# Kernel optimization log

Hardware: AMD Instinct MI355X
Metric: run time of the kernel (lower is better)

The kernel has to match this reference:

```python
import jax, jax.numpy as jnp
import numpy as np
import math

N, E, G = 20000, 160000, 256
H, L, R, LAT, TD = 128, 4, 64, 128, 64
CUT = 6.0
NTYPES = 101  # max_atomic_num=100 -> 101 rows, row 0 is padding


def _lin(key, fan_in, fan_out):
    kw, _ = jax.random.split(key)
    w = jax.random.normal(kw, (fan_in, fan_out), jnp.float32) / np.sqrt(fan_in).astype(np.float32)
    b = jnp.zeros((fan_out,), jnp.float32)
    return w, b


def _stack_lin(key, fan_in, fan_out):
    keys = jax.random.split(key, L)
    ws, bs = zip(*[_lin(k, fan_in, fan_out) for k in keys])
    return jnp.stack(ws), jnp.stack(bs)


def setup_inputs() -> dict:
    key = jax.random.key(0)
    ks = list(jax.random.split(key, 24))
    noisy_coords = jax.random.uniform(ks[0], (N, 3), jnp.float32)
    noisy_types = jax.random.randint(ks[1], (N,), 0, NTYPES)
    z = jax.random.normal(ks[2], (G, LAT), jnp.float32)
    t = jax.random.uniform(ks[3], (G,), jnp.float32) * 1000.0
    edge_index = jax.random.randint(ks[4], (2, E), 0, N)
    batch = jnp.sort(jax.random.randint(ks[5], (N,), 0, G))
    lattice = jnp.eye(3, dtype=jnp.float32)[None] * 5.0 + 0.1 * jax.random.normal(ks[6], (G, 3, 3), jnp.float32)
    offsets = jax.random.randint(ks[7], (E, 3), -1, 2).astype(jnp.float32)
    atom_embed = jax.random.normal(ks[8], (NTYPES, H), jnp.float32) * 0.02
    atom_embed = atom_embed.at[0].set(0.0)  # padding_idx=0
    z_w, z_b = _lin(ks[9], LAT, H)
    t_w, t_b = _lin(ks[10], TD, H)
    msg_w1, msg_b1 = _stack_lin(ks[11], H, H)
    msg_w2, msg_b2 = _stack_lin(ks[12], H, 3 * H)
    rbf_w, rbf_b = _stack_lin(ks[13], R, 3 * H)
    U = jax.random.normal(ks[14], (L, H, H), jnp.float32) / np.sqrt(H).astype(np.float32)
    V = jax.random.normal(ks[15], (L, H, H), jnp.float32) / np.sqrt(H).astype(np.float32)
    upd_w1, upd_b1 = _stack_lin(ks[16], 2 * H, H)
    upd_w2, upd_b2 = _stack_lin(ks[17], H, 3 * H)
    hc_w1, hc_b1 = _lin(ks[18], H, H)
    hc_w2, hc_b2 = _lin(ks[19], H, 3)
    ht_w1, ht_b1 = _lin(ks[20], H, H)
    ht_w2, ht_b2 = _lin(ks[21], H, NTYPES)
    return dict(noisy_coords=noisy_coords, noisy_types=noisy_types, z=z, t=t,
                edge_index=edge_index, batch=batch, lattice=lattice, offsets=offsets,
                atom_embed=atom_embed, z_w=z_w, z_b=z_b, t_w=t_w, t_b=t_b,
                msg_w1=msg_w1, msg_b1=msg_b1, msg_w2=msg_w2, msg_b2=msg_b2,
                rbf_w=rbf_w, rbf_b=rbf_b, U=U, V=V,
                upd_w1=upd_w1, upd_b1=upd_b1, upd_w2=upd_w2, upd_b2=upd_b2,
                hc_w1=hc_w1, hc_b1=hc_b1, hc_w2=hc_w2, hc_b2=hc_b2,
                ht_w1=ht_w1, ht_b1=ht_b1, ht_w2=ht_w2, ht_b2=ht_b2)


def reference(noisy_coords, noisy_types, z, t, edge_index, batch, lattice, offsets,
              atom_embed, z_w, z_b, t_w, t_b,
              msg_w1, msg_b1, msg_w2, msg_b2, rbf_w, rbf_b, U, V,
              upd_w1, upd_b1, upd_w2, upd_b2,
              hc_w1, hc_b1, hc_w2, hc_b2, ht_w1, ht_b1, ht_w2, ht_b2):
    n = noisy_coords.shape[0]
    src, dst = edge_index[0], edge_index[1]

    # node embeddings + conditioning
    s = atom_embed[noisy_types]                       # [N, H]
    v = jnp.zeros((n, 3, H), s.dtype)                 # [N, 3, H]
    half = TD // 2
    freqs = jnp.exp(-math.log(10000.0) * jnp.arange(half, dtype=jnp.float32) / (half - 1))
    emb = t[:, None] * freqs[None, :]                 # [G, TD/2]
    t_emb = jnp.concatenate([jnp.sin(emb), jnp.cos(emb)], axis=-1)  # [G, TD]
    cond = (z @ z_w + z_b)[batch] + (t_emb @ t_w + t_b)[batch]      # [N, H]

    # edge geometry: gather -> diff -> 3x3 matmul -> norm -> RBF -> normalize
    frac_diff = noisy_coords[dst] - noisy_coords[src] + offsets     # [E, 3]
    cart = jnp.einsum('ei,eij->ej', frac_diff, lattice[batch[src]]) # [E, 3]
    dist = jnp.maximum(jnp.sqrt(jnp.sum(cart * cart, -1)), 1e-8)    # clamp(min=1e-8)
    centers = jnp.linspace(0.0, CUT, R)
    gamma = jnp.float32(R / CUT)
    rbf = jnp.exp(-gamma * (dist[:, None] - centers[None, :]) ** 2) # [E, R]
    unit = cart / jnp.maximum(jnp.sqrt(jnp.sum(cart * cart, -1, keepdims=True)), 1e-12)

    # PaiNN layers (canonical message + update blocks)
    for l in range(L):
        s = s + cond
        # message block
        phi = jax.nn.silu(s @ msg_w1[l] + msg_b1[l]) @ msg_w2[l] + msg_b2[l]  # [N, 3H]
        filt = rbf @ rbf_w[l] + rbf_b[l]                                      # [E, 3H]
        x = phi[src] * filt
        ds, dv1, dv2 = jnp.split(x, 3, axis=-1)
        s = s + jax.ops.segment_sum(ds, dst, num_segments=n)
        vmsg = dv1[:, None, :] * v[src] + dv2[:, None, :] * unit[:, :, None]  # [E, 3, H]
        v = v + jax.ops.segment_sum(vmsg, dst, num_segments=n)
        # update block
        Uv = jnp.einsum('nch,hk->nck', v, U[l])
        Vv = jnp.einsum('nch,hk->nck', v, V[l])
        Vn = jnp.sqrt(jnp.sum(Vv * Vv, axis=1) + 1e-8)                        # [N, H]
        a = jax.nn.silu(jnp.concatenate([s, Vn], -1) @ upd_w1[l] + upd_b1[l]) @ upd_w2[l] + upd_b2[l]
        avv, asv, ass = jnp.split(a, 3, axis=-1)
        v = v + avv[:, None, :] * Uv
        s = s + asv * jnp.sum(Uv * Vv, axis=1) + ass

    coords_out = jax.nn.silu(s @ hc_w1 + hc_b1) @ hc_w2 + hc_b2   # [N, 3]
    type_out = jax.nn.silu(s @ ht_w1 + ht_b1) @ ht_w2 + ht_b2     # [N, 101]
    return coords_out, type_out
```

## Files before the change

### kernel.cpp

```cpp
#include <hip/hip_runtime.h>
#include <hip/hip_bf16.h>

#define HD 128
#define RD 64
#define H3 384

typedef float f32x4 __attribute__((ext_vector_type(4)));
typedef unsigned short us8 __attribute__((ext_vector_type(8)));
typedef __bf16 bf16x8 __attribute__((ext_vector_type(8)));

__device__ __forceinline__ float silu_f(float x) {
    return x / (1.0f + __expf(-x));
}
__device__ __forceinline__ unsigned short f2bf(float x) {
    __hip_bfloat16 h = __float2bfloat16(x);
    return *reinterpret_cast<unsigned short*>(&h);
}
__device__ __forceinline__ float bf2f(unsigned short u) {
    return __uint_as_float(((unsigned)u) << 16);
}
__device__ __forceinline__ f32x4 mfma3(us8 ah, us8 al, us8 bh, us8 bl, f32x4 c) {
    bf16x8 AH = __builtin_bit_cast(bf16x8, ah);
    bf16x8 AL = __builtin_bit_cast(bf16x8, al);
    bf16x8 BH = __builtin_bit_cast(bf16x8, bh);
    bf16x8 BL = __builtin_bit_cast(bf16x8, bl);
    c = __builtin_amdgcn_mfma_f32_16x16x32_bf16(AH, BH, c, 0, 0, 0);
    c = __builtin_amdgcn_mfma_f32_16x16x32_bf16(AH, BL, c, 0, 0, 0);
    c = __builtin_amdgcn_mfma_f32_16x16x32_bf16(AL, BH, c, 0, 0, 0);
    return c;
}

__global__ void wprep_kernel(const float* __restrict__ src,
                             unsigned short* __restrict__ dhi, unsigned short* __restrict__ dlo,
                             int K, int OUT, int sStride, int dStride, int nlay) {
    int total = K * OUT;
    for (int idx = blockIdx.x * blockDim.x + threadIdx.x; idx < total * nlay;
         idx += gridDim.x * blockDim.x) {
        int lyr = idx / total, r = idx % total;
        int o = r / K, k = r % K;
        float x = src[(size_t)lyr * sStride + (size_t)k * OUT + o];
        unsigned short hi = f2bf(x);
        unsigned short lo = f2bf(x - bf2f(hi));
        dhi[(size_t)lyr * dStride + (size_t)o * K + k] = hi;
        dlo[(size_t)lyr * dStride + (size_t)o * K + k] = lo;
    }
}

__global__ __launch_bounds__(128) void cond_kernel(const float* __restrict__ z, const float* __restrict__ t,
                            const float* __restrict__ z_w, const float* __restrict__ z_b,
                            const float* __restrict__ t_w, const float* __restrict__ t_b,
                            float* __restrict__ condG) {
    int g = blockIdx.x;
    int k = threadIdx.x;
    __shared__ float zr[128];
    __shared__ float te[64];
    zr[k] = z[g * 128 + k];
    if (k < 32) {
        float f = __expf(-9.2103403719761836f * (float)k / 31.0f);
        float e = t[g] * f;
        te[k] = sinf(e);
        te[32 + k] = cosf(e);
    }
    __syncthreads();
    float acc = z_b[k] + t_b[k];
    #pragma unroll 8
    for (int i = 0; i < 128; ++i) acc += zr[i] * z_w[i * 128 + k];
    #pragma unroll 8
    for (int i = 0; i < 64; ++i) acc += te[i] * t_w[i * 128 + k];
    condG[g * 128 + k] = acc;
}

__global__ void init_kernel(const int* __restrict__ types, const float* __restrict__ emb,
                            const float* __restrict__ condG, const int* __restrict__ batch,
                            float* __restrict__ s, int N_) {
    int i = blockIdx.x * blockDim.x + threadIdx.x;
    if (i < N_ * HD) {
        int n = i >> 7;
        int k = i & 127;
        s[i] = emb[types[n] * HD + k] + condG[batch[n] * 128 + k];
    }
}

__global__ void geom_kernel(const float* __restrict__ coords, const int* __restrict__ srcI,
                            const int* __restrict__ dstI, const int* __restrict__ batch,
                            const float* __restrict__ lattice, const float* __restrict__ offs,
                            float* __restrict__ dist, float* __restrict__ unit, int E_) {
    int e = blockIdx.x * blockDim.x + threadIdx.x;
    if (e >= E_) return;
    int sn = srcI[e], dn = dstI[e];
    float f0 = coords[dn * 3 + 0] - coords[sn * 3 + 0] + offs[e * 3 + 0];
    float f1 = coords[dn * 3 + 1] - coords[sn * 3 + 1] + offs[e * 3 + 1];
    float f2 = coords[dn * 3 + 2] - coords[sn * 3 + 2] + offs[e * 3 + 2];
    const float* Lg = lattice + batch[sn] * 9;
    float c0 = f0 * Lg[0] + f1 * Lg[3] + f2 * Lg[6];
    float c1 = f0 * Lg[1] + f1 * Lg[4] + f2 * Lg[7];
    float c2 = f0 * Lg[2] + f1 * Lg[5] + f2 * Lg[8];
    float nrm = sqrtf(c0 * c0 + c1 * c1 + c2 * c2);
    dist[e] = fmaxf(nrm, 1e-8f);
    float inv = 1.0f / fmaxf(nrm, 1e-12f);
    unit[e * 3 + 0] = c0 * inv;
    unit[e * 3 + 1] = c1 * inv;
    unit[e * 3 + 2] = c2 * inv;
}

__global__ void hist_kernel(const int* __restrict__ dstI, int* __restrict__ cnt, int E_) {
    int e = blockIdx.x * blockDim.x + threadIdx.x;
    if (e < E_) atomicAdd(&cnt[dstI[e]], 1);
}

__global__ __launch_bounds__(1024) void scan_kernel(const int* __restrict__ cnt, int* __restrict__ cur, int n) {
    __shared__ int tmp[1024];
    __shared__ int carry_s;
    if (threadIdx.x == 0) carry_s = 0;
    __syncthreads();
    for (int base = 0; base < n; base += 1024) {
        int i = base + threadIdx.x;
        int x = (i < n) ? cnt[i] : 0;
        tmp[threadIdx.x] = x;
        __syncthreads();
        for (int off = 1; off < 1024; off <<= 1) {
            int y = (threadIdx.x >= off) ? tmp[threadIdx.x - off] : 0;
            __syncthreads();
            tmp[threadIdx.x] += y;
            __syncthreads();
        }
        if (i < n) cur[i] = carry_s + tmp[threadIdx.x] - x;
        __syncthreads();
        if (threadIdx.x == 0) carry_s += tmp[1023];
        __syncthreads();
    }
}

__global__ void scatter_kernel(const int* __restrict__ srcI, const int* __restrict__ dstI,
                               const float* __restrict__ dist, const float* __restrict__ unit,
                               int* __restrict__ cur,
                               float* __restrict__ dist_s, float* __restrict__ unit_s,
                               int* __restrict__ src_s, int* __restrict__ dst_s, int E_) {
    int e = blockIdx.x * blockDim.x + threadIdx.x;
    if (e >= E_) return;
    int d = dstI[e];
    int p = atomicAdd(&cur[d], 1);
    dist_s[p] = dist[e];
    unit_s[p * 3 + 0] = unit[e * 3 + 0];
    unit_s[p * 3 + 1] = unit[e * 3 + 1];
    unit_s[p * 3 + 2] = unit[e * 3 + 2];
    src_s[p] = srcI[e];
    dst_s[p] = d;
}

#define PSA 136
__global__ __launch_bounds__(256, 2) void phi_mfma(
    const float* __restrict__ s,
    const unsigned short* __restrict__ w1h, const unsigned short* __restrict__ w1l,
    const float* __restrict__ b1,
    const unsigned short* __restrict__ w2h, const unsigned short* __restrict__ w2l,
    const float* __restrict__ b2,
    float* __restrict__ phi, int N_) {
    __shared__ unsigned short Ah[32 * PSA], Al[32 * PSA], Hh[32 * PSA], Hl[32 * PSA];
    const int tid = threadIdx.x;
    const int n0 = blockIdx.x * 32;
    for (int idx = tid; idx < 32 * 128; idx += 256) {
        int j = idx >> 7, k = idx & 127;
        int n = n0 + j; if (n >= N_) n = N_ - 1;
        float x = s[(size_t)n * 128 + k];
        unsigned short h = f2bf(x);
        Ah[j * PSA + k] = h;
        Al[j * PSA + k] = f2bf(x - bf2f(h));
    }
    __syncthreads();
    const int w = tid >> 6, l = tid & 63;
    const int lr = l & 15, lk = (l >> 4) << 3, rg0 = (l >> 4) << 2;
    const f32x4 zero4 = {0.0f, 0.0f, 0.0f, 0.0f};
    f32x4 acc1[2][2];
    #pragma unroll
    for (int rt = 0; rt < 2; ++rt)
        #pragma unroll
        for (int ci = 0; ci < 2; ++ci) acc1[rt][ci] = zero4;
    #pragma unroll
    for (int kt = 0; kt < 4; ++kt) {
        int kk = kt * 32 + lk;
        us8 bh[2], bl[2], ah[2], alo[2];
        #pragma unroll
        for (int ci = 0; ci < 2; ++ci) {
            int col = (w * 2 + ci) * 16 + lr;
            bh[ci] = *(const us8*)(w1h + (size_t)col * 128 + kk);
            bl[ci] = *(const us8*)(w1l + (size_t)col * 128 + kk);
        }
        #pragma unroll
        for (int rt = 0; rt < 2; ++rt) {
            ah[rt]  = *(const us8*)(Ah + (rt * 16 + lr) * PSA + kk);
            alo[rt] = *(const us8*)(Al + (rt * 16 + lr) * PSA + kk);
        }
        #pragma unroll
        for (int rt = 0; rt < 2; ++rt)
            #pragma unroll
            for (int ci = 0; ci < 2; ++ci)
                acc1[rt][ci] = mfma3(ah[rt], alo[rt], bh[ci], bl[ci], acc1[rt][ci]);
    }
    #pragma unroll
    for (int rt = 0; rt < 2; ++rt)
        #pragma unroll
        for (int ci = 0; ci < 2; ++ci) {
            int col = (w * 2 + ci) * 16 + lr;
            float bb = b1[col];
            #pragma unroll
            for (int rg = 0; rg < 4; ++rg) {
                int j = rt * 16 + rg0 + rg;
                float hv = silu_f(acc1[rt][ci][rg] + bb);
                unsigned short hh = f2bf(hv);
                Hh[j * PSA + col] = hh;
                Hl[j * PSA + col] = f2bf(hv - bf2f(hh));
            }
        }
    __syncthreads();
    f32x4 acc2[2][6];
    #pragma unroll
    for (int rt = 0; rt < 2; ++rt)
        #pragma unroll
        for (int ci = 0; ci < 6; ++ci) acc2[rt][ci] = zero4;
    #pragma unroll
    for (int kt = 0; kt < 4; ++kt) {
        int kk = kt * 32 + lk;
        us8 ah[2], alo[2];
        #pragma unroll
        for (int rt = 0; rt < 2; ++rt) {
            ah[rt]  = *(const us8*)(Hh + (rt * 16 + lr) * PSA + kk);
            alo[rt] = *(const us8*)(Hl + (rt * 16 + lr) * PSA + kk);
        }
        #pragma unroll
        for (int ci = 0; ci < 6; ++ci) {
            int col = (w * 6 + ci) * 16 + lr;
            us8 bh = *(const us8*)(w2h + (size_t)col * 128 + kk);
            us8 bl = *(const us8*)(w2l + (size_t)col * 128 + kk);
            #pragma unroll
            for (int rt = 0; rt < 2; ++rt)
                acc2[rt][ci] = mfma3(ah[rt], alo[rt], bh, bl, acc2[rt][ci]);
        }
    }
    #pragma unroll
    for (int rt = 0; rt < 2; ++rt)
        #pragma unroll
        for (int ci = 0; ci < 6; ++ci) {
            int col = (w * 6 + ci) * 16 + lr;
            float bb = b2[col];
            #pragma unroll
            for (int rg = 0; rg < 4; ++rg) {
                int j = rt * 16 + rg0 + rg;
                int n = n0 + j;
                if (n < N_) phi[(size_t)n * 384 + col] = acc2[rt][ci][rg] + bb;
            }
        }
}

__global__ __launch_bounds__(256, 2) void upd_mfma(
    const unsigned short* __restrict__ Uh, const unsigned short* __restrict__ Ul,
    const unsigned short* __restrict__ Vh, const unsigned short* __restrict__ Vl,
    const unsigned short* __restrict__ w1h, const unsigned short* __restrict__ w1l,
    const float* __restrict__ b1,
    const unsigned short* __restrict__ w2h, const unsigned short* __restrict__ w2l,
    const float* __restrict__ b2,
    float* __restrict__ s, float* __restrict__ v, const float* __restrict__ dv,
    const float* __restrict__ condG, const int* __restrict__ batch, int addcond, int N_) {
    __shared__ unsigned short SMA[2 * 48 * 136];
    __shared__ float UvL[48 * 132];
    __shared__ float VvL[48 * 132];
    unsigned short* VNh = SMA;
    unsigned short* VNl = SMA + 48 * 136;
    unsigned short* A1h = SMA;
    unsigned short* A1l = SMA + 16 * 264;
    unsigned short* a1h = SMA + 32 * 264;
    unsigned short* a1l = SMA + 32 * 264 + 16 * 136;
    float* o384 = VvL;
    const int tid = threadIdx.x;
    const int n0 = blockIdx.x * 16;
    for (int idx = tid; idx < 48 * 128; idx += 256) {
        int r = idx >> 7, k = idx & 127;
        int c = r >> 4, j = r & 15;
        int n = n0 + j; if (n >= N_) n = N_ - 1;
        size_t off = (size_t)n * 384 + c * 128 + k;
        float x = v[off] + dv[off];
        unsigned short h = f2bf(x);
        VNh[r * 136 + k] = h;
        VNl[r * 136 + k] = f2bf(x - bf2f(h));
    }
    __syncthreads();
    const int w = tid >> 6, l = tid & 63;
    const int lr = l & 15, lk = (l >> 4) << 3, rg0 = (l >> 4) << 2;
    const f32x4 zero4 = {0.0f, 0.0f, 0.0f, 0.0f};
    {
        f32x4 acc[3][2];
        #pragma unroll
        for (int rt = 0; rt < 3; ++rt) { acc[rt][0] = zero4; acc[rt][1] = zero4; }
        #pragma unroll
        for (int kt = 0; kt < 4; ++kt) {
            int kk = kt * 32 + lk;
            us8 bh[2], bl[2];
            #pragma unroll
            for (int ci = 0; ci < 2; ++ci) {
                int col = (w * 2 + ci) * 16 + lr;
                bh[ci] = *(const us8*)(Uh + (size_t)col * 128 + kk);
                bl[ci] = *(const us8*)(Ul + (size_t)col * 128 + kk);
            }
            #pragma unroll
            for (int rt = 0; rt < 3; ++rt) {
                us8 ah  = *(const us8*)(VNh + (rt * 16 + lr) * 136 + kk);
                us8 alo = *(const us8*)(VNl + (rt * 16 + lr) * 136 + kk);
                #pragma unroll
                for (int ci = 0; ci < 2; ++ci)
                    acc[rt][ci] = mfma3(ah, alo, bh[ci], bl[ci], acc[rt][ci]);
            }
        }
        #pragma unroll
        for (int rt = 0; rt < 3; ++rt)
            #pragma unroll
            for (int ci = 0; ci < 2; ++ci) {
                int col = (w * 2 + ci) * 16 + lr;
                #pragma unroll
                for (int rg = 0; rg < 4; ++rg)
                    UvL[(rt * 16 + rg0 + rg) * 132 + col] = acc[rt][ci][rg];
            }
        #pragma unroll
        for (int rt = 0; rt < 3; ++rt) { acc[rt][0] = zero4; acc[rt][1] = zero4; }
        #pragma unroll
        for (int kt = 0; kt < 4; ++kt) {
            int kk = kt * 32 + lk;
            us8 bh[2], bl[2];
            #pragma unroll
            for (int ci = 0; ci < 2; ++ci) {
                int col = (w * 2 + ci) * 16 + lr;
                bh[ci] = *(const us8*)(Vh + (size_t)col * 128 + kk);
                bl[ci] = *(const us8*)(Vl + (size_t)col * 128 + kk);
            }
            #pragma unroll
            for (int rt = 0; rt < 3; ++rt) {
                us8 ah  = *(const us8*)(VNh + (rt * 16 + lr) * 136 + kk);
                us8 alo = *(const us8*)(VNl + (rt * 16 + lr) * 136 + kk);
                #pragma unroll
                for (int ci = 0; ci < 2; ++ci)
                    acc[rt][ci] = mfma3(ah, alo, bh[ci], bl[ci], acc[rt][ci]);
            }
        }
        #pragma unroll
        for (int rt = 0; rt < 3; ++rt)
            #pragma unroll
            for (int ci = 0; ci < 2; ++ci) {
                int col = (w * 2 + ci) * 16 + lr;
                #pragma unroll
                for (int rg = 0; rg < 4; ++rg)
                    VvL[(rt * 16 + rg0 + rg) * 132 + col] = acc[rt][ci][rg];
            }
    }
    __syncthreads();
    float dotr[8];
    {
        int k = tid & 127;
        int jb = (tid >> 7) * 8;
        #pragma unroll
        for (int i = 0; i < 8; ++i) {
            int j = jb + i;
            float uv0 = UvL[j * 132 + k], uv1 = UvL[(16 + j) * 132 + k], uv2 = UvL[(32 + j) * 132 + k];
            float vv0 = VvL[j * 132 + k], vv1 = VvL[(16 + j) * 132 + k], vv2 = VvL[(32 + j) * 132 + k];
            dotr[i] = uv0 * vv0 + uv1 * vv1 + uv2 * vv2;
            float vnv = sqrtf(vv0 * vv0 + vv1 * vv1 + vv2 * vv2 + 1e-8f);
            int n = n0 + j; if (n >= N_) n = N_ - 1;
            float sv = s[(size_t)n * 128 + k];
            unsigned short h1 = f2bf(sv);
            A1h[j * 264 + k] = h1;
            A1l[j * 264 + k] = f2bf(sv - bf2f(h1));
            unsigned short h2 = f2bf(vnv);
            A1h[j * 264 + 128 + k] = h2;
            A1l[j * 264 + 128 + k] = f2bf(vnv - bf2f(h2));
        }
    }
    __syncthreads();
    {
        f32x4 acc[2]; acc[0] = zero4; acc[1] = zero4;
        #pragma unroll
        for (int kt = 0; kt < 8; ++kt) {
            int kk = kt * 32 + lk;
            us8 ah  = *(const us8*)(A1h + lr * 264 + kk);
            us8 alo = *(const us8*)(A1l + lr * 264 + kk);
            #pragma unroll
            for (int ci = 0; ci < 2; ++ci) {
                int col = (w * 2 + ci) * 16 + lr;
                us8 bh = *(const us8*)(w1h + (size_t)col * 256 + kk);
                us8 bl = *(const us8*)(w1l + (size_t)col * 256 + kk);
                acc[ci] = mfma3(ah, alo, bh, bl, acc[ci]);
            }
        }
        #pragma unroll
        for (int ci = 0; ci < 2; ++ci) {
            int col = (w * 2 + ci) * 16 + lr;
            float bb = b1[col];
            #pragma unroll
            for (int rg = 0; rg < 4; ++rg) {
                int j = rg0 + rg;
                float hv = silu_f(acc[ci][rg] + bb);
                unsigned short hh = f2bf(hv);
                a1h[j * 136 + col] = hh;
                a1l[j * 136 + col] = f2bf(hv - bf2f(hh));
            }
        }
    }
    __syncthreads();
    {
        f32x4 acc[6];
        #pragma unroll
        for (int ci = 0; ci < 6; ++ci) acc[ci] = zero4;
        #pragma unroll
        for (int kt = 0; kt < 4; ++kt) {
            int kk = kt * 32 + lk;
            us8 ah  = *(const us8*)(a1h + lr * 136 + kk);
            us8 alo = *(const us8*)(a1l + lr * 136 + kk);
            #pragma unroll
            for (int ci = 0; ci < 6; ++ci) {
                int col = (w * 6 + ci) * 16 + lr;
                us8 bh = *(const us8*)(w2h + (size_t)col * 128 + kk);
                us8 bl = *(const us8*)(w2l + (size_t)col * 128 + kk);
                acc[ci] = mfma3(ah, alo, bh, bl, acc[ci]);
            }
        }
        #pragma unroll
        for (int ci = 0; ci < 6; ++ci) {
            int col = (w * 6 + ci) * 16 + lr;
            float bb = b2[col];
            #pragma unroll
            for (int rg = 0; rg < 4; ++rg) {
                int j = rg0 + rg;
                o384[j * 388 + col] = acc[ci][rg] + bb;
            }
        }
    }
    __syncthreads();
    {
        int k = tid & 127;
        int jb = (tid >> 7) * 8;
        #pragma unroll
        for (int i = 0; i < 8; ++i) {
            int j = jb + i;
            int n = n0 + j;
            if (n >= N_) continue;
            float a0  = o384[j * 388 + k];
            float aH  = o384[j * 388 + 128 + k];
            float a2v = o384[j * 388 + 256 + k];
            #pragma unroll
            for (int c = 0; c < 3; ++c) {
                size_t off = (size_t)n * 384 + c * 128 + k;
                v[off] = v[off] + dv[off] + a0 * UvL[(c * 16 + j) * 132 + k];
            }
            float cadd = addcond ? condG[(size_t)batch[n] * 128 + k] : 0.0f;
            s[(size_t)n * 128 + k] += aH * dotr[i] + a2v + cadd;
        }
    }
}

#define EB 64
__global__ __launch_bounds__(256, 2) void edge_mfma(
    const float* __restrict__ phi, const float* __restrict__ v,
    const float* __restrict__ dist_s, const float* __restrict__ unit_s,
    const int* __restrict__ src_s, const int* __restrict__ dst_s,
    const unsigned short* __restrict__ rwh, const unsigned short* __restrict__ rwl,
    const float* __restrict__ rb,
    float* __restrict__ s, float* __restrict__ dv, int E_) {
    __shared__ unsigned short Rh[64 * 72];
    __shared__ unsigned short Rl[64 * 72];
    __shared__ float filt[32 * 388];
    const int tid = threadIdx.x;
    const int e0 = blockIdx.x * EB;
    #pragma unroll
    for (int i = 0; i < 16; ++i) {
        int idx = i * 256 + tid;
        int e = idx >> 6, r = idx & 63;
        float val = 0.0f;
        int ge = e0 + e;
        if (ge < E_) {
            float d = dist_s[ge];
            float c = 6.0f * (float)r / 63.0f;
            float tt = d - c;
            val = __expf(-(64.0f / 6.0f) * tt * tt);
        }
        unsigned short h = f2bf(val);
        Rh[e * 72 + r] = h;
        Rl[e * 72 + r] = f2bf(val - bf2f(h));
    }
    __syncthreads();
    const int w = tid >> 6, l = tid & 63;
    const int lr = l & 15, lk = (l >> 4) << 3, rg0 = (l >> 4) << 2;
    const f32x4 zero4 = {0.0f, 0.0f, 0.0f, 0.0f};
    f32x4 acc[4][6];
    #pragma unroll
    for (int mt = 0; mt < 4; ++mt)
        #pragma unroll
        for (int nt = 0; nt < 6; ++nt) acc[mt][nt] = zero4;
    #pragma unroll
    for (int kt = 0; kt < 2; ++kt) {
        int kk = kt * 32 + lk;
        us8 ah[4], al[4];
        #pragma unroll
        for (int mt = 0; mt < 4; ++mt) {
            ah[mt] = *(const us8*)(Rh + (mt * 16 + lr) * 72 + kk);
            al[mt] = *(const us8*)(Rl + (mt * 16 + lr) * 72 + kk);
        }
        #pragma unroll
        for (int nt = 0; nt < 6; ++nt) {
            int col = w * 96 + nt * 16 + lr;
            us8 bh = *(const us8*)(rwh + (size_t)col * 64 + kk);
            us8 bl = *(const us8*)(rwl + (size_t)col * 64 + kk);
            #pragma unroll
            for (int mt = 0; mt < 4; ++mt)
                acc[mt][nt] = mfma3(ah[mt], al[mt], bh, bl, acc[mt][nt]);
        }
    }
    const int sub = tid >> 7;
    const int col = tid & 127;
    float b0 = rb[col], b1 = rb[128 + col], b2 = rb[256 + col];
    float as = 0.0f, ad0 = 0.0f, ad1 = 0.0f, ad2 = 0.0f;
    int rd = -1;
    #pragma unroll
    for (int ch = 0; ch < 2; ++ch) {
        __syncthreads();
        #pragma unroll
        for (int mt = 0; mt < 2; ++mt)
            #pragma unroll
            for (int nt = 0; nt < 6; ++nt) {
                int c2 = w * 96 + nt * 16 + lr;
                #pragma unroll
                for (int rg = 0; rg < 4; ++rg)
                    filt[(mt * 16 + rg0 + rg) * 388 + c2] = acc[2 * ch + mt][nt][rg];
            }
        __syncthreads();
        int le0 = ch * 32 + sub * 16;
        for (int i = 0; i < 16; ++i) {
            int e = e0 + le0 + i;
            if (e >= E_) break;
            int dn = dst_s[e];
            if (dn != rd) {
                if (rd >= 0) {
                    atomicAdd(&s[(size_t)rd * 128 + col], as);
                    atomicAdd(&dv[(size_t)rd * 384 + col], ad0);
                    atomicAdd(&dv[(size_t)rd * 384 + 128 + col], ad1);
                    atomicAdd(&dv[(size_t)rd * 384 + 256 + col], ad2);
                }
                as = ad0 = ad1 = ad2 = 0.0f;
                rd = dn;
            }
            int sn = src_s[e];
            int fr = sub * 16 + i;
            float f0 = filt[fr * 388 + col] + b0;
            float f1 = filt[fr * 388 + 128 + col] + b1;
            float f2v = filt[fr * 388 + 256 + col] + b2;
            const float* phr = phi + (size_t)sn * 384;
            const float* vr = v + (size_t)sn * 384;
            float x0 = phr[col] * f0;
            float x1 = phr[128 + col] * f1;
            float x2 = phr[256 + col] * f2v;
            float u0 = unit_s[e * 3 + 0], u1 = unit_s[e * 3 + 1], u2 = unit_s[e * 3 + 2];
            as += x0;
            ad0 += x1 * vr[col] + x2 * u0;
            ad1 += x1 * vr[128 + col] + x2 * u1;
            ad2 += x1 * vr[256 + col] + x2 * u2;
        }
    }
    if (rd >= 0) {
        atomicAdd(&s[(size_t)rd * 128 + col], as);
        atomicAdd(&dv[(size_t)rd * 384 + col], ad0);
        atomicAdd(&dv[(size_t)rd * 384 + 128 + col], ad1);
        atomicAdd(&dv[(size_t)rd * 384 + 256 + col], ad2);
    }
}

#define HPB 8
__global__ __launch_bounds__(128, 4) void heads_kernel(
    const float* __restrict__ s,
    const float* __restrict__ hc_w1, const float* __restrict__ hc_b1,
    const float* __restrict__ hc_w2, const float* __restrict__ hc_b2,
    const float* __restrict__ ht_w1, const float* __restrict__ ht_b1,
    const float* __restrict__ ht_w2, const float* __restrict__ ht_b2,
    float* __restrict__ outc, float* __restrict__ outt, int N_) {
    int n0 = blockIdx.x * HPB;
    int k = threadIdx.x;
    __shared__ float sr[HPB][128];
    __shared__ float h1[HPB][128];
    __shared__ float h2[HPB][128];
    #pragma unroll
    for (int j = 0; j < HPB; ++j) {
        int n = n0 + j;
        sr[j][k] = (n < N_) ? s[(size_t)n * 128 + k] : 0.0f;
    }
    __syncthreads();
    float a[HPB], b[HPB];
    #pragma unroll
    for (int j = 0; j < HPB; ++j) { a[j] = hc_b1[k]; b[j] = ht_b1[k]; }
    for (int h = 0; h < 128; h += 4) {
        float wa0 = hc_w1[h * 128 + k],       wa1 = hc_w1[(h + 1) * 128 + k];
        float wa2 = hc_w1[(h + 2) * 128 + k], wa3 = hc_w1[(h + 3) * 128 + k];
        float wb0 = ht_w1[h * 128 + k],       wb1 = ht_w1[(h + 1) * 128 + k];
        float wb2 = ht_w1[(h + 2) * 128 + k], wb3 = ht_w1[(h + 3) * 128 + k];
        #pragma unroll
        for (int j = 0; j < HPB; ++j) {
            const float4 x = *reinterpret_cast<const float4*>(&sr[j][h]);
            a[j] = fmaf(x.w, wa3, fmaf(x.z, wa2, fmaf(x.y, wa1, fmaf(x.x, wa0, a[j]))));
            b[j] = fmaf(x.w, wb3, fmaf(x.z, wb2, fmaf(x.y, wb1, fmaf(x.x, wb0, b[j]))));
        }
    }
    #pragma unroll
    for (int j = 0; j < HPB; ++j) {
        h1[j][k] = silu_f(a[j]);
        h2[j][k] = silu_f(b[j]);
    }
    __syncthreads();
    if (k < 101) {
        for (int j = 0; j < HPB; ++j) {
            int n = n0 + j;
            if (n >= N_) break;
            float c = ht_b2[k];
            #pragma unroll 4
            for (int h = 0; h < 128; ++h) c += h2[j][h] * ht_w2[h * 101 + k];
            outt[(size_t)n * 101 + k] = c;
        }
    }
    if (k < 3) {
        for (int j = 0; j < HPB; ++j) {
            int n = n0 + j;
            if (n >= N_) break;
            float c = hc_b2[k];
            #pragma unroll 4
            for (int h = 0; h < 128; ++h) c += h1[j][h] * hc_w2[h * 3 + k];
            outc[(size_t)n * 3 + k] = c;
        }
    }
}

extern "C" void kernel_launch(void* const* d_in, const int* in_sizes, int n_in,
                              void* d_out, int out_size, void* d_ws, size_t ws_size,
                              hipStream_t stream) {
    const float* coords  = (const float*)d_in[0];
    const int*   types   = (const int*)d_in[1];
    const float* z       = (const float*)d_in[2];
    const float* t       = (const float*)d_in[3];
    const int*   eidx    = (const int*)d_in[4];
    const int*   batch   = (const int*)d_in[5];
    const float* lattice = (const float*)d_in[6];
    const float* offs    = (const float*)d_in[7];
    const float* aemb    = (const float*)d_in[8];
    const float* z_w     = (const float*)d_in[9];
    const float* z_b     = (const float*)d_in[10];
    const float* t_w     = (const float*)d_in[11];
    const float* t_b     = (const float*)d_in[12];
    const float* msg_w1  = (const float*)d_in[13];
    const float* msg_b1  = (const float*)d_in[14];
    const float* msg_w2  = (const float*)d_in[15];
    const float* msg_b2  = (const float*)d_in[16];
    const float* rbf_w   = (const float*)d_in[17];
    const float* rbf_b   = (const float*)d_in[18];
    const float* Um      = (const float*)d_in[19];
    const float* Vm      = (const float*)d_in[20];
    const float* upd_w1  = (const float*)d_in[21];
    const float* upd_b1  = (const float*)d_in[22];
    const float* upd_w2  = (const float*)d_in[23];
    const float* upd_b2  = (const float*)d_in[24];
    const float* hc_w1   = (const float*)d_in[25];
    const float* hc_b1   = (const float*)d_in[26];
    const float* hc_w2   = (const float*)d_in[27];
    const float* hc_b2   = (const float*)d_in[28];
    const float* ht_w1   = (const float*)d_in[29];
    const float* ht_b1   = (const float*)d_in[30];
    const float* ht_w2   = (const float*)d_in[31];
    const float* ht_b2   = (const float*)d_in[32];

    const int N = in_sizes[1];
    const int G = in_sizes[3];
    const int E = in_sizes[4] / 2;
    const int* srcI = eidx;
    const int* dstI = eidx + E;

    char* ws = (char*)d_ws;
    auto alloc = [&](size_t bytes) {
        char* p = ws;
        ws += (bytes + 255) & ~(size_t)255;
        return p;
    };
    float* s_buf   = (float*)alloc((size_t)N * HD * 4);
    float* v_buf   = (float*)alloc((size_t)N * H3 * 4);
    float* dv_buf  = (float*)alloc((size_t)N * H3 * 4);
    float* phi_buf = (float*)alloc((size_t)N * H3 * 4);
    float* condG   = (float*)alloc((size_t)G * HD * 4);
    float* dist_s  = (float*)alloc((size_t)E * 4);
    float* unit_s  = (float*)alloc((size_t)E * 3 * 4);
    int*   src_s   = (int*)alloc((size_t)E * 4);
    int*   dst_s   = (int*)alloc((size_t)E * 4);
    int*   cur     = (int*)alloc((size_t)N * 4);
    const size_t LS = 409600;
    unsigned short* wpr = (unsigned short*)alloc((size_t)4 * LS * 2);
    float* dist_t  = phi_buf;
    float* unit_t  = phi_buf + E;

    hipMemsetAsync(v_buf, 0, (size_t)N * H3 * 4, stream);
    hipMemsetAsync(cur, 0, (size_t)N * 4, stream);
    cond_kernel<<<G, 128, 0, stream>>>(z, t, z_w, z_b, t_w, t_b, condG);
    init_kernel<<<(N * HD + 255) / 256, 256, 0, stream>>>(types, aemb, condG, batch, s_buf, N);
    geom_kernel<<<(E + 255) / 256, 256, 0, stream>>>(coords, srcI, dstI, batch, lattice, offs, dist_t, unit_t, E);
    hist_kernel<<<(E + 255) / 256, 256, 0, stream>>>(dstI, cur, E);
    {
        int* cnt2 = (int*)(phi_buf + 4 * (size_t)E);
        hipMemcpyAsync(cnt2, cur, (size_t)N * 4, hipMemcpyDeviceToDevice, stream);
        scan_kernel<<<1, 1024, 0, stream>>>(cnt2, cur, N);
    }
    scatter_kernel<<<(E + 255) / 256, 256, 0, stream>>>(srcI, dstI, dist_t, unit_t, cur,
                                                        dist_s, unit_s, src_s, dst_s, E);
    wprep_kernel<<<256, 256, 0, stream>>>(msg_w1, wpr + 0,      wpr + 16384,  128, 128, 16384, (int)LS, 4);
    wprep_kernel<<<768, 256, 0, stream>>>(msg_w2, wpr + 32768,  wpr + 81920,  128, 384, 49152, (int)LS, 4);
    wprep_kernel<<<512, 256, 0, stream>>>(upd_w1, wpr + 131072, wpr + 163840, 256, 128, 32768, (int)LS, 4);
    wprep_kernel<<<768, 256, 0, stream>>>(upd_w2, wpr + 196608, wpr + 245760, 128, 384, 49152, (int)LS, 4);
    wprep_kernel<<<256, 256, 0, stream>>>(Um,     wpr + 294912, wpr + 311296, 128, 128, 16384, (int)LS, 4);
    wprep_kernel<<<256, 256, 0, stream>>>(Vm,     wpr + 327680, wpr + 344064, 128, 128, 16384, (int)LS, 4);
    wprep_kernel<<<384, 256, 0, stream>>>(rbf_w,  wpr + 360448, wpr + 385024, 64,  384, 24576, (int)LS, 4);

    int eblocks = (E + EB - 1) / EB;
    int pblocks = (N + 31) / 32;
    int ublocks = (N + 15) / 16;
    int hblocks = (N + HPB - 1) / HPB;
    for (int l = 0; l < 4; ++l) {
        const unsigned short* L = wpr + (size_t)l * LS;
        phi_mfma<<<pblocks, 256, 0, stream>>>(s_buf,
                L + 0, L + 16384, msg_b1 + (size_t)l * HD,
                L + 32768, L + 81920, msg_b2 + (size_t)l * H3,
                phi_buf, N);
        hipMemsetAsync(dv_buf, 0, (size_t)N * H3 * 4, stream);
        edge_mfma<<<eblocks, 256, 0, stream>>>(phi_buf, v_buf, dist_s, unit_s, src_s, dst_s,
                                               L + 360448, L + 385024,
                                               rbf_b + (size_t)l * H3,
                                               s_buf, dv_buf, E);
        upd_mfma<<<ublocks, 256, 0, stream>>>(
                L + 294912, L + 311296, L + 327680, L + 344064,
                L + 131072, L + 163840, upd_b1 + (size_t)l * HD,
                L + 196608, L + 245760, upd_b2 + (size_t)l * H3,
                s_buf, v_buf, dv_buf, condG, batch, (l < 3) ? 1 : 0, N);
    }
    heads_kernel<<<hblocks, 128, 0, stream>>>(s_buf, hc_w1, hc_b1, hc_w2, hc_b2,
                                        ht_w1, ht_b1, ht_w2, ht_b2,
                                        (float*)d_out, (float*)d_out + (size_t)N * 3, N);
}
```

Measured before the change: 1.625 ms.

## Shrink edge kernel LDS by aliasing RBF tiles and staging filter in 16-row chunks

The edge kernel's LDS footprint is reduced by aliasing the bf16 RBF hi/lo buffers onto the filter staging buffer and staging the filter in four chunks of 16 edges instead of two of 32. The RBF tile is also written directly in MFMA fragment order, so each lane loads its A operand contiguously without padded strides. This targets higher occupancy through lower shared memory use, at the cost of twice as many barrier rounds in the scatter phase.

```diff
diff --git a/kernel.cpp b/kernel.cpp
--- a/kernel.cpp
+++ b/kernel.cpp
@@ -462,17 +462,22 @@
     const unsigned short* __restrict__ rwh, const unsigned short* __restrict__ rwl,
     const float* __restrict__ rb,
     float* __restrict__ s, float* __restrict__ dv, int E_) {
-    __shared__ unsigned short Rh[64 * 72];
-    __shared__ unsigned short Rl[64 * 72];
-    __shared__ float filt[32 * 388];
+    __shared__ float filt[16 * 388];
+    unsigned short* Rh = (unsigned short*)filt;
+    unsigned short* Rl = Rh + 4096;
     const int tid = threadIdx.x;
     const int e0 = blockIdx.x * EB;
     #pragma unroll
-    for (int i = 0; i < 16; ++i) {
-        int idx = i * 256 + tid;
-        int e = idx >> 6, r = idx & 63;
+    for (int it = 0; it < 16; ++it) {
+        int idx = it * 256 + tid;
+        int i = idx & 7;
+        int l2 = (idx >> 3) & 63;
+        int mt = (idx >> 9) & 3;
+        int kt = idx >> 11;
+        int edge = mt * 16 + (l2 & 15);
+        int r = kt * 32 + ((l2 >> 4) << 3) + i;
         float val = 0.0f;
-        int ge = e0 + e;
+        int ge = e0 + edge;
         if (ge < E_) {
             float d = dist_s[ge];
             float c = 6.0f * (float)r / 63.0f;
@@ -480,12 +485,12 @@
             val = __expf(-(64.0f / 6.0f) * tt * tt);
         }
         unsigned short h = f2bf(val);
-        Rh[e * 72 + r] = h;
-        Rl[e * 72 + r] = f2bf(val - bf2f(h));
+        Rh[idx] = h;
+        Rl[idx] = f2bf(val - bf2f(h));
     }
     __syncthreads();
     const int w = tid >> 6, l = tid & 63;
-    const int lr = l & 15, lk = (l >> 4) << 3, rg0 = (l >> 4) << 2;
+    const int lr = l & 15, rg0 = (l >> 4) << 2;
     const f32x4 zero4 = {0.0f, 0.0f, 0.0f, 0.0f};
     f32x4 acc[4][6];
     #pragma unroll
@@ -494,13 +499,14 @@
         for (int nt = 0; nt < 6; ++nt) acc[mt][nt] = zero4;
     #pragma unroll
     for (int kt = 0; kt < 2; ++kt) {
-        int kk = kt * 32 + lk;
         us8 ah[4], al[4];
         #pragma unroll
         for (int mt = 0; mt < 4; ++mt) {
-            ah[mt] = *(const us8*)(Rh + (mt * 16 + lr) * 72 + kk);
-            al[mt] = *(const us8*)(Rl + (mt * 16 + lr) * 72 + kk);
-        }
+            int base = ((kt * 4 + mt) * 64 + l) * 8;
+            ah[mt] = *(const us8*)(Rh + base);
+            al[mt] = *(const us8*)(Rl + base);
+        }
+        int kk = kt * 32 + ((l >> 4) << 3);
         #pragma unroll
         for (int nt = 0; nt < 6; ++nt) {
             int col = w * 96 + nt * 16 + lr;
@@ -517,20 +523,18 @@
     float as = 0.0f, ad0 = 0.0f, ad1 = 0.0f, ad2 = 0.0f;
     int rd = -1;
     #pragma unroll
-    for (int ch = 0; ch < 2; ++ch) {
+    for (int ch = 0; ch < 4; ++ch) {
         __syncthreads();
         #pragma unroll
-        for (int mt = 0; mt < 2; ++mt)
-            #pragma unroll
-            for (int nt = 0; nt < 6; ++nt) {
-                int c2 = w * 96 + nt * 16 + lr;
-                #pragma unroll
-                for (int rg = 0; rg < 4; ++rg)
-                    filt[(mt * 16 + rg0 + rg) * 388 + c2] = acc[2 * ch + mt][nt][rg];
-            }
+        for (int nt = 0; nt < 6; ++nt) {
+            int c2 = w * 96 + nt * 16 + lr;
+            #pragma unroll
+            for (int rg = 0; rg < 4; ++rg)
+                filt[(rg0 + rg) * 388 + c2] = acc[ch][nt][rg];
+        }
         __syncthreads();
-        int le0 = ch * 32 + sub * 16;
-        for (int i = 0; i < 16; ++i) {
+        int le0 = ch * 16 + sub * 8;
+        for (int i = 0; i < 8; ++i) {
             int e = e0 + le0 + i;
             if (e >= E_) break;
             int dn = dst_s[e];
@@ -545,7 +549,7 @@
                 rd = dn;
             }
             int sn = src_s[e];
-            int fr = sub * 16 + i;
+            int fr = sub * 8 + i;
             float f0 = filt[fr * 388 + col] + b0;
             float f1 = filt[fr * 388 + 128 + col] + b1;
             float f2v = filt[fr * 388 + 256 + col] + b2;
```

Result: no change. 1.620 ms (-0.3%).
